# Kernel tuning notes

Hardware: AMD Instinct MI355X
Metric: run time of the kernel (lower is better)

## Reference

```python
import jax, jax.numpy as jnp
import numpy as np

DIM = 768
HEADS = 12
HEAD_DIM = DIM // HEADS
SCALE = HEAD_DIM ** (-0.5)


def setup_inputs() -> dict:
    key = jax.random.key(0)
    k1, k2, k3, k4 = jax.random.split(key, 4)
    B, N = 2, 48 * 48
    x = jax.random.normal(k1, (B, N, DIM), dtype=jnp.float32)
    qkv_w = jax.random.normal(k2, (3 * DIM, DIM), dtype=jnp.float32) * (DIM ** -0.5)
    proj_w = jax.random.normal(k3, (DIM, DIM), dtype=jnp.float32) * (DIM ** -0.5)
    proj_b = jax.random.normal(k4, (DIM,), dtype=jnp.float32) * 0.02
    return {"x": x, "H": 48, "W": 48, "qkv_w": qkv_w, "proj_w": proj_w, "proj_b": proj_b}


def reference(x, H, W, qkv_w, proj_w, proj_b):
    B, N, C = x.shape
    h, d = HEADS, HEAD_DIM
    # qkv linear (no bias): [B,N,3C], then split into per-head q,k,v [B,h,N,d]
    qkv = jnp.einsum('bnc,fc->bnf', x, qkv_w)
    qkv = qkv.reshape(B, N, 3, h, d).transpose(2, 0, 3, 1, 4)
    q, k, v = qkv[0], qkv[1], qkv[2]
    attn = jnp.einsum('bhnd,bhmd->bhnm', q, k) * SCALE  # [B,h,N,N]
    attn = jax.nn.softmax(attn, axis=-1)
    out = jnp.einsum('bhnm,bhmd->bhnd', attn, v)  # [B,h,N,d]
    out = out.transpose(0, 2, 1, 3).reshape(B, N, C)
    out = jnp.einsum('bnc,fc->bnf', out, proj_w) + proj_b
    return out
```

## Files before the change

### kernel.cpp

```cpp
#include <hip/hip_runtime.h>

#define B_    2
#define N_    2304
#define C_    768
#define HEADS 12
#define D_    64
#define F3    2304
#define M_    (B_*N_)
#define SPLITS 2
#define KSPAN (N_/SPLITS)
#define QSCALE 0.18033688011112042f

typedef __attribute__((ext_vector_type(8)))  short bfrag;
typedef __attribute__((ext_vector_type(4)))  float ffrag;
typedef __attribute__((ext_vector_type(16))) float ffrag16;
typedef __attribute__((ext_vector_type(4)))  unsigned ufrag;
typedef __attribute__((ext_vector_type(2)))  unsigned uint2v;

__device__ __forceinline__ short f2bf(float f) {
    unsigned u = __float_as_uint(f);
    u += 0x7fff + ((u >> 16) & 1);
    return (short)(u >> 16);
}

__device__ __forceinline__ void gl2lds16(const void* g, void* l) {
    __builtin_amdgcn_global_load_lds(
        (const __attribute__((address_space(1))) void*)g,
        (__attribute__((address_space(3))) void*)l, 16, 0, 0);
}

__device__ __forceinline__ void wait_vm4() { asm volatile("s_waitcnt vmcnt(4)" ::: "memory"); }
__device__ __forceinline__ void wait_vm0() { asm volatile("s_waitcnt vmcnt(0)" ::: "memory"); }

__device__ __forceinline__ unsigned pktrunc(float a, float b) {
    return __builtin_amdgcn_perm(__float_as_uint(a), __float_as_uint(b),
                                 0x03020706u);
}

__global__ __launch_bounds__(256) void cast_all(const float* __restrict__ x,
                                                const float* __restrict__ qw,
                                                const float* __restrict__ pw,
                                                short* __restrict__ dst) {
    const int nx4 = (M_*C_)/4, nq4 = (F3*C_)/4, np4 = (C_*C_)/4;
    int i = blockIdx.x * 256 + threadIdx.x;
    if (i >= nx4 + nq4 + np4) return;
    const float* src; int off;
    if (i < nx4)            { src = x;  off = i; }
    else if (i < nx4 + nq4) { src = qw; off = i - nx4; }
    else                    { src = pw; off = i - nx4 - nq4; }
    float4 v = ((const float4*)src)[off];
    short4 o;
    o.x = f2bf(v.x); o.y = f2bf(v.y); o.z = f2bf(v.z); o.w = f2bf(v.w);
    ((short4*)dst)[i] = o;
}

__global__ __launch_bounds__(256) void qkv_gemm(const short* __restrict__ xb,
                                                const short* __restrict__ wb,
                                                short* __restrict__ Qb,
                                                short* __restrict__ Kb,
                                                short* __restrict__ Vtb) {
    __shared__ short As[2][128*32];
    __shared__ short Bs[2][128*32];
    const int t = threadIdx.x;
    const int w = t >> 6, lane = t & 63;
    const int quad = lane >> 4, l15 = lane & 15;
    const int wr = w >> 1, wc = w & 1;

    const int nwg = gridDim.x * gridDim.y;
    const int bid = blockIdx.y * gridDim.x + blockIdx.x;
    const int swz = (bid & 7) * (nwg >> 3) + (bid >> 3);
    const int m0 = (swz / gridDim.x) * 128, f0 = (swz % gridDim.x) * 128;

    const int srow = lane >> 2;
    const int skk  = (lane & 3) * 8;

    ffrag acc[4][4] = {};

    #pragma unroll
    for (int r = 0; r < 2; ++r) {
        int seg = r*4 + w;
        int row = seg*16 + srow;
        gl2lds16(xb + (size_t)(m0+row)*C_ + skk, As[0] + seg*512);
        gl2lds16(wb + (size_t)(f0+row)*C_ + skk, Bs[0] + seg*512);
    }

    const int NKT = C_/32;
    for (int kt = 0; kt < NKT; ++kt) {
        const int cur = kt & 1;
        if (kt + 1 < NKT) {
            const int k0n = (kt+1)*32;
            #pragma unroll
            for (int r = 0; r < 2; ++r) {
                int seg = r*4 + w;
                int row = seg*16 + srow;
                gl2lds16(xb + (size_t)(m0+row)*C_ + k0n + skk, As[cur^1] + seg*512);
                gl2lds16(wb + (size_t)(f0+row)*C_ + k0n + skk, Bs[cur^1] + seg*512);
            }
            wait_vm4();
        } else {
            wait_vm0();
        }
        __builtin_amdgcn_s_barrier();

        bfrag af[4], bf[4];
        #pragma unroll
        for (int i = 0; i < 4; ++i)
            af[i] = *(const bfrag*)(As[cur] + (wr*64 + i*16 + l15)*32 + quad*8);
        #pragma unroll
        for (int j = 0; j < 4; ++j)
            bf[j] = *(const bfrag*)(Bs[cur] + (wc*64 + j*16 + l15)*32 + quad*8);
        #pragma unroll
        for (int i = 0; i < 4; ++i)
            #pragma unroll
            for (int j = 0; j < 4; ++j)
                acc[i][j] = __builtin_amdgcn_mfma_f32_16x16x32_bf16(af[i], bf[j], acc[i][j], 0, 0, 0);
        __builtin_amdgcn_s_barrier();
    }

    const int b   = m0 / N_;
    const int seg = f0 + wc*64;
    const int which = seg / C_;
    const int head  = (seg - which*C_) >> 6;
    const int bh    = b*HEADS + head;
    const int nbase = (m0 - b*N_) + wr*64 + quad*4;

    if (which == 0) {
        #pragma unroll
        for (int i = 0; i < 4; ++i) {
            int n0 = nbase + i*16;
            #pragma unroll
            for (int j = 0; j < 4; ++j) {
                int d = j*16 + l15;
                #pragma unroll
                for (int r = 0; r < 4; ++r)
                    Qb[((size_t)bh*N_ + n0 + r)*D_ + d] = f2bf(acc[i][j][r] * QSCALE);
            }
        }
    } else if (which == 1) {
        #pragma unroll
        for (int i = 0; i < 4; ++i) {
            int n0 = nbase + i*16;
            #pragma unroll
            for (int j = 0; j < 4; ++j) {
                int d = j*16 + l15;
                #pragma unroll
                for (int r = 0; r < 4; ++r)
                    Kb[((size_t)bh*N_ + n0 + r)*D_ + d] = f2bf(acc[i][j][r]);
            }
        }
    } else {
        #pragma unroll
        for (int i = 0; i < 4; ++i) {
            int n0 = nbase + i*16;
            #pragma unroll
            for (int j = 0; j < 4; ++j) {
                int d = j*16 + l15;
                short4 vv;
                vv.x = f2bf(acc[i][j][0]);
                vv.y = f2bf(acc[i][j][1]);
                vv.z = f2bf(acc[i][j][2]);
                vv.w = f2bf(acc[i][j][3]);
                *(short4*)(Vtb + ((size_t)bh*D_ + d)*N_ + n0) = vv;
            }
        }
    }
}

__global__ __launch_bounds__(256, 4) void attn_mfma(const short* __restrict__ Qb,
                                                    const short* __restrict__ Kb,
                                                    const short* __restrict__ Vtb,
                                                    float* __restrict__ Opart,
                                                    float* __restrict__ lpart) {
    __shared__ short lds[16384];
    const int t = threadIdx.x;
    const int w = t >> 6, lane = t & 63;
    const int l31 = lane & 31, hi = lane >> 5;

    const int nwg = gridDim.x * gridDim.y;
    const int fid = blockIdx.y * gridDim.x + blockIdx.x;
    const int swz = (fid & 7) * (nwg >> 3) + (fid >> 3);
    const int bh  = swz / gridDim.x;
    const int q0  = (swz - bh * gridDim.x) * 128;

    const int split = blockIdx.z;
    const int kbase = split * KSPAN;
    const size_t base = (size_t)bh * N_ * D_;
    const int lrow = lane >> 3;
    const int lc   = (lane & 7) ^ lrow;

    short* Qs = lds + 8192;

    #pragma unroll
    for (int r = 0; r < 4; ++r) {
        int s = r*4 + w;
        gl2lds16(Qb + base + (size_t)(q0 + s*8 + lrow)*D_ + lc*8, Qs + s*512);
    }
    #pragma unroll
    for (int r = 0; r < 2; ++r) {
        int s = r*4 + w;
        int row = s*8 + lrow;
        gl2lds16(Kb  + base + (size_t)(kbase+row)*D_ + lc*8,    lds + s*512);
        gl2lds16(Vtb + (size_t)(bh*D_ + row)*N_ + kbase + lc*8, lds + 4096 + s*512);
    }
    __syncthreads();

    bfrag qf[4];
    {
        int row = w*32 + l31, r7 = row & 7;
        #pragma unroll
        for (int kc = 0; kc < 4; ++kc)
            qf[kc] = *(const bfrag*)(Qs + row*64 + ((kc*2 + hi) ^ r7)*8);
    }
    __syncthreads();

    bfrag vones;
    #pragma unroll
    for (int j = 0; j < 8; ++j) vones[j] = (short)0x3f80;

    ffrag16 oacc[2], lfr;
    #pragma unroll
    for (int r = 0; r < 16; ++r) { oacc[0][r] = 0.f; oacc[1][r] = 0.f; lfr[r] = 0.f; }

    const int NT = KSPAN / 64;
    for (int ti = 0; ti < NT; ++ti) {
        const int cur = ti & 1;
        const short* Kc = lds + cur*8192;
        const short* Vc = Kc + 4096;

        if (ti + 1 < NT) {
            short* Kn = lds + (cur^1)*8192;
            const int k0n = kbase + (ti+1)*64;
            #pragma unroll
            for (int r = 0; r < 2; ++r) {
                int s = r*4 + w;
                int row = s*8 + lrow;
                gl2lds16(Kb  + base + (size_t)(k0n+row)*D_ + lc*8,    Kn + s*512);
                gl2lds16(Vtb + (size_t)(bh*D_ + row)*N_ + k0n + lc*8, Kn + 4096 + s*512);
            }
            wait_vm4();
        } else {
            wait_vm0();
        }
        __builtin_amdgcn_s_barrier();

        ufrag pfr[4];
        #pragma unroll
        for (int kt = 0; kt < 2; ++kt) {
            ffrag16 s;
            #pragma unroll
            for (int r = 0; r < 16; ++r) s[r] = 0.f;
            int row = kt*32 + l31, r7 = row & 7;
            __builtin_amdgcn_s_setprio(1);
            #pragma unroll
            for (int kc = 0; kc < 4; ++kc) {
                bfrag kf = *(const bfrag*)(Kc + row*64 + ((kc*2 + hi) ^ r7)*8);
                s = __builtin_amdgcn_mfma_f32_32x32x16_bf16(kf, qf[kc], s, 0, 0, 0);
            }
            __builtin_amdgcn_s_setprio(0);
            #pragma unroll
            for (int r = 0; r < 16; ++r)
                s[r] = __builtin_amdgcn_exp2f(s[r]);
            unsigned q01_0 = pktrunc(s[0],  s[1]),  q23_0 = pktrunc(s[2],  s[3]);
            unsigned q01_1 = pktrunc(s[4],  s[5]),  q23_1 = pktrunc(s[6],  s[7]);
            unsigned q01_2 = pktrunc(s[8],  s[9]),  q23_2 = pktrunc(s[10], s[11]);
            unsigned q01_3 = pktrunc(s[12], s[13]), q23_3 = pktrunc(s[14], s[15]);
            uint2v e0 = __builtin_amdgcn_permlane32_swap(q01_0, q01_1, false, false);
            uint2v e1 = __builtin_amdgcn_permlane32_swap(q23_0, q23_1, false, false);
            uint2v e2 = __builtin_amdgcn_permlane32_swap(q01_2, q01_3, false, false);
            uint2v e3 = __builtin_amdgcn_permlane32_swap(q23_2, q23_3, false, false);
            ufrag lo, hif;
            lo[0]  = e0[0]; lo[1]  = e1[0]; lo[2]  = e0[1]; lo[3]  = e1[1];
            hif[0] = e2[0]; hif[1] = e3[0]; hif[2] = e2[1]; hif[3] = e3[1];
            pfr[kt*2]     = lo;
            pfr[kt*2 + 1] = hif;
        }

        __builtin_amdgcn_s_setprio(1);
        #pragma unroll
        for (int kc = 0; kc < 4; ++kc) {
            bfrag pf = __builtin_bit_cast(bfrag, pfr[kc]);
            #pragma unroll
            for (int dt = 0; dt < 2; ++dt) {
                int row = dt*32 + l31, r7 = row & 7;
                bfrag vf = *(const bfrag*)(Vc + row*64 + ((kc*2 + hi) ^ r7)*8);
                oacc[dt] = __builtin_amdgcn_mfma_f32_32x32x16_bf16(pf, vf, oacc[dt], 0, 0, 0);
            }
            lfr = __builtin_amdgcn_mfma_f32_32x32x16_bf16(pf, vones, lfr, 0, 0, 0);
        }
        __builtin_amdgcn_s_setprio(0);
        __builtin_amdgcn_s_barrier();
    }

    const int b = bh / HEADS, head = bh - b*HEADS;
    float* Op = Opart + (size_t)split * M_ * C_;
    float* lp = lpart + (size_t)split * (B_*HEADS) * N_;

    if (l31 == 0) {
        #pragma unroll
        for (int r = 0; r < 16; ++r) {
            int n = q0 + w*32 + (r & 3) + 8*(r >> 2) + 4*hi;
            lp[bh*N_ + n] = lfr[r];
        }
    }

    #pragma unroll
    for (int dt = 0; dt < 2; ++dt)
        #pragma unroll
        for (int r = 0; r < 16; ++r) {
            int n = q0 + w*32 + (r & 3) + 8*(r >> 2) + 4*hi;
            int c = head*D_ + dt*32 + l31;
            Op[((size_t)b*N_ + n)*C_ + c] = oacc[dt][r];
        }
}

__global__ __launch_bounds__(256) void attn_merge(const float* __restrict__ Opart,
                                                  const float* __restrict__ lpart,
                                                  short* __restrict__ Ob) {
    int i = blockIdx.x * 256 + threadIdx.x;
    int m = i / (C_/4);
    int c = (i - m*(C_/4)) * 4;
    int b = m / N_, n = m - b*N_;
    int bh = b*HEADS + (c >> 6);
    float4 o0 = ((const float4*)Opart)[i];
    float4 o1 = ((const float4*)(Opart + (size_t)M_*C_))[i];
    float l = lpart[bh*N_ + n] + lpart[(B_*HEADS)*N_ + bh*N_ + n];
    float inv = 1.f / l;
    short4 o;
    o.x = f2bf((o0.x + o1.x) * inv);
    o.y = f2bf((o0.y + o1.y) * inv);
    o.z = f2bf((o0.z + o1.z) * inv);
    o.w = f2bf((o0.w + o1.w) * inv);
    ((short4*)Ob)[i] = o;
}

__global__ __launch_bounds__(256) void proj_gemm(const short* __restrict__ Ab,
                                                 const short* __restrict__ wb,
                                                 const float* __restrict__ bias,
                                                 float* __restrict__ out) {
    __shared__ short As[2][128*32];
    __shared__ short Bs[2][128*32];
    const int t = threadIdx.x;
    const int w = t >> 6, lane = t & 63;
    const int quad = lane >> 4, l15 = lane & 15;
    const int wr = w >> 1, wc = w & 1;

    const int nwg = gridDim.x * gridDim.y;
    const int bid = blockIdx.y * gridDim.x + blockIdx.x;
    const int swz = (bid & 7) * (nwg >> 3) + (bid >> 3);
    const int m0 = (swz / gridDim.x) * 128, f0 = (swz % gridDim.x) * 128;

    const int srow = lane >> 2;
    const int skk  = (lane & 3) * 8;

    ffrag acc[4][4] = {};

    #pragma unroll
    for (int r = 0; r < 2; ++r) {
        int seg = r*4 + w;
        int row = seg*16 + srow;
        gl2lds16(Ab + (size_t)(m0+row)*C_ + skk, As[0] + seg*512);
        gl2lds16(wb + (size_t)(f0+row)*C_ + skk, Bs[0] + seg*512);
    }

    const int NKT = C_/32;
    for (int kt = 0; kt < NKT; ++kt) {
        const int cur = kt & 1;
        if (kt + 1 < NKT) {
            const int k0n = (kt+1)*32;
            #pragma unroll
            for (int r = 0; r < 2; ++r) {
                int seg = r*4 + w;
                int row = seg*16 + srow;
                gl2lds16(Ab + (size_t)(m0+row)*C_ + k0n + skk, As[cur^1] + seg*512);
                gl2lds16(wb + (size_t)(f0+row)*C_ + k0n + skk, Bs[cur^1] + seg*512);
            }
            wait_vm4();
        } else {
            wait_vm0();
        }
        __builtin_amdgcn_s_barrier();

        bfrag af[4], bf[4];
        #pragma unroll
        for (int i = 0; i < 4; ++i)
            af[i] = *(const bfrag*)(As[cur] + (wr*64 + i*16 + l15)*32 + quad*8);
        #pragma unroll
        for (int j = 0; j < 4; ++j)
            bf[j] = *(const bfrag*)(Bs[cur] + (wc*64 + j*16 + l15)*32 + quad*8);
        #pragma unroll
        for (int i = 0; i < 4; ++i)
            #pragma unroll
            for (int j = 0; j < 4; ++j)
                acc[i][j] = __builtin_amdgcn_mfma_f32_16x16x32_bf16(af[i], bf[j], acc[i][j], 0, 0, 0);
        __builtin_amdgcn_s_barrier();
    }

    #pragma unroll
    for (int i = 0; i < 4; ++i) {
        int mbase = m0 + wr*64 + i*16 + quad*4;
        #pragma unroll
        for (int j = 0; j < 4; ++j) {
            int f = f0 + wc*64 + j*16 + l15;
            float bv = bias[f];
            #pragma unroll
            for (int r = 0; r < 4; ++r)
                out[(size_t)(mbase + r)*C_ + f] = acc[i][j][r] + bv;
        }
    }
}

extern "C" void kernel_launch(void* const* d_in, const int* in_sizes, int n_in,
                              void* d_out, int out_size, void* d_ws, size_t ws_size,
                              hipStream_t stream) {
    const float* x      = (const float*)d_in[0];
    const float* qkv_w  = (const float*)d_in[3];
    const float* proj_w = (const float*)d_in[4];
    const float* proj_b = (const float*)d_in[5];
    float* out = (float*)d_out;

    const size_t nx = (size_t)M_ * C_;
    const size_t nq = (size_t)F3 * C_;
    const size_t np = (size_t)C_ * C_;
    short* xb  = (short*)d_ws;
    short* qwb = xb  + nx;
    short* pwb = qwb + nq;
    short* Qb  = pwb + np;
    short* Kb  = Qb  + nx;
    short* Vtb = Kb  + nx;
    short* Ob  = Vtb + nx;
    float* Opart = (float*)(Ob + nx);
    float* lpart = Opart + (size_t)SPLITS * M_ * C_;

    const int ncast4 = (int)((nx + nq + np) / 4);
    cast_all<<<dim3((ncast4 + 255)/256), 256, 0, stream>>>(x, qkv_w, proj_w, xb);

    qkv_gemm<<<dim3(F3/128, M_/128), 256, 0, stream>>>(xb, qwb, Qb, Kb, Vtb);
    attn_mfma<<<dim3(N_/128, B_*HEADS, SPLITS), 256, 0, stream>>>(Qb, Kb, Vtb, Opart, lpart);
    attn_merge<<<dim3(((int)(nx/4) + 255)/256), 256, 0, stream>>>(Opart, lpart, Ob);
    proj_gemm<<<dim3(C_/128, M_/128), 256, 0, stream>>>(Ob, pwb, proj_b, out);
}
```

Baseline: 194.4 us.

## Software-pipeline attention loop to overlap QK/exp of next half with PV MFMAs

Restructures the attention inner loop so the second half-tile's QK^T, exp and packing, along with its V fragment loads into registers, are carried across the barrier and consumed in the next iteration. The PV MFMAs of the previous half then interleave with the current tile's QK and exp work. The first tile is peeled as a prologue and a final PV step is added as an epilogue. The goal is to hide exp/VALU latency behind matrix ops, at the cost of extra live registers (P and V fragments) under launch_bounds(256,4).

```diff
diff --git a/kernel.cpp b/kernel.cpp
--- a/kernel.cpp
+++ b/kernel.cpp
@@ -166,6 +166,83 @@
     }
 }
 
+
+__device__ __forceinline__ void qkpack(const short* Kc, const bfrag* qf,
+                                       int kt, int l31, int hi,
+                                       ufrag& u0, ufrag& u1) {
+    ffrag16 s;
+    #pragma unroll
+    for (int r = 0; r < 16; ++r) s[r] = 0.f;
+    int row = kt*32 + l31, r7 = row & 7;
+    __builtin_amdgcn_s_setprio(1);
+    #pragma unroll
+    for (int kc = 0; kc < 4; ++kc) {
+        bfrag kf = *(const bfrag*)(Kc + row*64 + ((kc*2 + hi) ^ r7)*8);
+        s = __builtin_amdgcn_mfma_f32_32x32x16_bf16(kf, qf[kc], s, 0, 0, 0);
+    }
+    __builtin_amdgcn_s_setprio(0);
+    #pragma unroll
+    for (int r = 0; r < 16; ++r)
+        s[r] = __builtin_amdgcn_exp2f(s[r]);
+    unsigned q01_0 = pktrunc(s[0],  s[1]),  q23_0 = pktrunc(s[2],  s[3]);
+    unsigned q01_1 = pktrunc(s[4],  s[5]),  q23_1 = pktrunc(s[6],  s[7]);
+    unsigned q01_2 = pktrunc(s[8],  s[9]),  q23_2 = pktrunc(s[10], s[11]);
+    unsigned q01_3 = pktrunc(s[12], s[13]), q23_3 = pktrunc(s[14], s[15]);
+    uint2v e0 = __builtin_amdgcn_permlane32_swap(q01_0, q01_1, false, false);
+    uint2v e1 = __builtin_amdgcn_permlane32_swap(q23_0, q23_1, false, false);
+    uint2v e2 = __builtin_amdgcn_permlane32_swap(q01_2, q01_3, false, false);
+    uint2v e3 = __builtin_amdgcn_permlane32_swap(q23_2, q23_3, false, false);
+    ufrag lo, hif;
+    lo[0]  = e0[0]; lo[1]  = e1[0]; lo[2]  = e0[1]; lo[3]  = e1[1];
+    hif[0] = e2[0]; hif[1] = e3[0]; hif[2] = e2[1]; hif[3] = e3[1];
+    u0 = lo; u1 = hif;
+}
+
+__device__ __forceinline__ void pv_lds(ufrag u0, ufrag u1, const short* Vc,
+                                       int kt, int l31, int hi, bfrag vones,
+                                       ffrag16& o0, ffrag16& o1, ffrag16& lf) {
+    int r0 = l31, r7a = r0 & 7;
+    int r1 = 32 + l31, r7b = r1 & 7;
+    bfrag p0 = __builtin_bit_cast(bfrag, u0);
+    bfrag p1 = __builtin_bit_cast(bfrag, u1);
+    int kcA = kt*2, kcB = kt*2 + 1;
+    bfrag vA0 = *(const bfrag*)(Vc + r0*64 + ((kcA*2 + hi) ^ r7a)*8);
+    bfrag vA1 = *(const bfrag*)(Vc + r1*64 + ((kcA*2 + hi) ^ r7b)*8);
+    bfrag vB0 = *(const bfrag*)(Vc + r0*64 + ((kcB*2 + hi) ^ r7a)*8);
+    bfrag vB1 = *(const bfrag*)(Vc + r1*64 + ((kcB*2 + hi) ^ r7b)*8);
+    o0 = __builtin_amdgcn_mfma_f32_32x32x16_bf16(p0, vA0, o0, 0, 0, 0);
+    o1 = __builtin_amdgcn_mfma_f32_32x32x16_bf16(p0, vA1, o1, 0, 0, 0);
+    lf = __builtin_amdgcn_mfma_f32_32x32x16_bf16(p0, vones, lf, 0, 0, 0);
+    o0 = __builtin_amdgcn_mfma_f32_32x32x16_bf16(p1, vB0, o0, 0, 0, 0);
+    o1 = __builtin_amdgcn_mfma_f32_32x32x16_bf16(p1, vB1, o1, 0, 0, 0);
+    lf = __builtin_amdgcn_mfma_f32_32x32x16_bf16(p1, vones, lf, 0, 0, 0);
+}
+
+__device__ __forceinline__ void pv_reg(ufrag u0, ufrag u1,
+                                       bfrag v0, bfrag v1, bfrag v2, bfrag v3,
+                                       bfrag vones,
+                                       ffrag16& o0, ffrag16& o1, ffrag16& lf) {
+    bfrag p0 = __builtin_bit_cast(bfrag, u0);
+    bfrag p1 = __builtin_bit_cast(bfrag, u1);
+    o0 = __builtin_amdgcn_mfma_f32_32x32x16_bf16(p0, v0, o0, 0, 0, 0);
+    o1 = __builtin_amdgcn_mfma_f32_32x32x16_bf16(p0, v1, o1, 0, 0, 0);
+    lf = __builtin_amdgcn_mfma_f32_32x32x16_bf16(p0, vones, lf, 0, 0, 0);
+    o0 = __builtin_amdgcn_mfma_f32_32x32x16_bf16(p1, v2, o0, 0, 0, 0);
+    o1 = __builtin_amdgcn_mfma_f32_32x32x16_bf16(p1, v3, o1, 0, 0, 0);
+    lf = __builtin_amdgcn_mfma_f32_32x32x16_bf16(p1, vones, lf, 0, 0, 0);
+}
+
+__device__ __forceinline__ void vload4(const short* Vc, int kt, int l31, int hi,
+                                       bfrag& v0, bfrag& v1, bfrag& v2, bfrag& v3) {
+    int r0 = l31, r7a = r0 & 7;
+    int r1 = 32 + l31, r7b = r1 & 7;
+    int kcA = kt*2, kcB = kt*2 + 1;
+    v0 = *(const bfrag*)(Vc + r0*64 + ((kcA*2 + hi) ^ r7a)*8);
+    v1 = *(const bfrag*)(Vc + r1*64 + ((kcA*2 + hi) ^ r7b)*8);
+    v2 = *(const bfrag*)(Vc + r0*64 + ((kcB*2 + hi) ^ r7a)*8);
+    v3 = *(const bfrag*)(Vc + r1*64 + ((kcB*2 + hi) ^ r7b)*8);
+}
+
 __global__ __launch_bounds__(256, 4) void attn_mfma(const short* __restrict__ Qb,
                                                     const short* __restrict__ Kb,
                                                     const short* __restrict__ Vtb,
@@ -217,12 +294,37 @@
     #pragma unroll
     for (int j = 0; j < 8; ++j) vones[j] = (short)0x3f80;
 
-    ffrag16 oacc[2], lfr;
-    #pragma unroll
-    for (int r = 0; r < 16; ++r) { oacc[0][r] = 0.f; oacc[1][r] = 0.f; lfr[r] = 0.f; }
+    ffrag16 oacc0, oacc1, lfr;
+    #pragma unroll
+    for (int r = 0; r < 16; ++r) { oacc0[r] = 0.f; oacc1[r] = 0.f; lfr[r] = 0.f; }
 
     const int NT = KSPAN / 64;
-    for (int ti = 0; ti < NT; ++ti) {
+
+    ufrag pP0, pP1;
+    bfrag vP0, vP1, vP2, vP3;
+
+    {
+        const int k0n = kbase + 64;
+        #pragma unroll
+        for (int r = 0; r < 2; ++r) {
+            int s = r*4 + w;
+            int row = s*8 + lrow;
+            gl2lds16(Kb  + base + (size_t)(k0n+row)*D_ + lc*8,    lds + 8192 + s*512);
+            gl2lds16(Vtb + (size_t)(bh*D_ + row)*N_ + k0n + lc*8, lds + 12288 + s*512);
+        }
+        const short* Kc = lds;
+        const short* Vc = lds + 4096;
+        ufrag a0, a1;
+        qkpack(Kc, qf, 0, l31, hi, a0, a1);
+        __builtin_amdgcn_s_setprio(1);
+        pv_lds(a0, a1, Vc, 0, l31, hi, vones, oacc0, oacc1, lfr);
+        __builtin_amdgcn_s_setprio(0);
+        qkpack(Kc, qf, 1, l31, hi, pP0, pP1);
+        vload4(Vc, 1, l31, hi, vP0, vP1, vP2, vP3);
+        __builtin_amdgcn_s_barrier();
+    }
+
+    for (int ti = 1; ti < NT; ++ti) {
         const int cur = ti & 1;
         const short* Kc = lds + cur*8192;
         const short* Vc = Kc + 4096;
@@ -243,53 +345,18 @@
         }
         __builtin_amdgcn_s_barrier();
 
-        ufrag pfr[4];
-        #pragma unroll
-        for (int kt = 0; kt < 2; ++kt) {
-            ffrag16 s;
-            #pragma unroll
-            for (int r = 0; r < 16; ++r) s[r] = 0.f;
-            int row = kt*32 + l31, r7 = row & 7;
-            __builtin_amdgcn_s_setprio(1);
-            #pragma unroll
-            for (int kc = 0; kc < 4; ++kc) {
-                bfrag kf = *(const bfrag*)(Kc + row*64 + ((kc*2 + hi) ^ r7)*8);
-                s = __builtin_amdgcn_mfma_f32_32x32x16_bf16(kf, qf[kc], s, 0, 0, 0);
-            }
-            __builtin_amdgcn_s_setprio(0);
-            #pragma unroll
-            for (int r = 0; r < 16; ++r)
-                s[r] = __builtin_amdgcn_exp2f(s[r]);
-            unsigned q01_0 = pktrunc(s[0],  s[1]),  q23_0 = pktrunc(s[2],  s[3]);
-            unsigned q01_1 = pktrunc(s[4],  s[5]),  q23_1 = pktrunc(s[6],  s[7]);
-            unsigned q01_2 = pktrunc(s[8],  s[9]),  q23_2 = pktrunc(s[10], s[11]);
-            unsigned q01_3 = pktrunc(s[12], s[13]), q23_3 = pktrunc(s[14], s[15]);
-            uint2v e0 = __builtin_amdgcn_permlane32_swap(q01_0, q01_1, false, false);
-            uint2v e1 = __builtin_amdgcn_permlane32_swap(q23_0, q23_1, false, false);
-            uint2v e2 = __builtin_amdgcn_permlane32_swap(q01_2, q01_3, false, false);
-            uint2v e3 = __builtin_amdgcn_permlane32_swap(q23_2, q23_3, false, false);
-            ufrag lo, hif;
-            lo[0]  = e0[0]; lo[1]  = e1[0]; lo[2]  = e0[1]; lo[3]  = e1[1];
-            hif[0] = e2[0]; hif[1] = e3[0]; hif[2] = e2[1]; hif[3] = e3[1];
-            pfr[kt*2]     = lo;
-            pfr[kt*2 + 1] = hif;
-        }
-
+        ufrag a0, a1;
+        qkpack(Kc, qf, 0, l31, hi, a0, a1);
         __builtin_amdgcn_s_setprio(1);
-        #pragma unroll
-        for (int kc = 0; kc < 4; ++kc) {
-            bfrag pf = __builtin_bit_cast(bfrag, pfr[kc]);
-            #pragma unroll
-            for (int dt = 0; dt < 2; ++dt) {
-                int row = dt*32 + l31, r7 = row & 7;
-                bfrag vf = *(const bfrag*)(Vc + row*64 + ((kc*2 + hi) ^ r7)*8);
-                oacc[dt] = __builtin_amdgcn_mfma_f32_32x32x16_bf16(pf, vf, oacc[dt], 0, 0, 0);
-            }
-            lfr = __builtin_amdgcn_mfma_f32_32x32x16_bf16(pf, vones, lfr, 0, 0, 0);
-        }
+        pv_reg(pP0, pP1, vP0, vP1, vP2, vP3, vones, oacc0, oacc1, lfr);
+        pv_lds(a0, a1, Vc, 0, l31, hi, vones, oacc0, oacc1, lfr);
         __builtin_amdgcn_s_setprio(0);
-        __builtin_amdgcn_s_barrier();
-    }
+        qkpack(Kc, qf, 1, l31, hi, pP0, pP1);
+        vload4(Vc, 1, l31, hi, vP0, vP1, vP2, vP3);
+        __builtin_amdgcn_s_barrier();
+    }
+
+    pv_reg(pP0, pP1, vP0, vP1, vP2, vP3, vones, oacc0, oacc1, lfr);
 
     const int b = bh / HEADS, head = bh - b*HEADS;
     float* Op = Opart + (size_t)split * M_ * C_;
@@ -304,13 +371,12 @@
     }
 
     #pragma unroll
-    for (int dt = 0; dt < 2; ++dt)
-        #pragma unroll
-        for (int r = 0; r < 16; ++r) {
-            int n = q0 + w*32 + (r & 3) + 8*(r >> 2) + 4*hi;
-            int c = head*D_ + dt*32 + l31;
-            Op[((size_t)b*N_ + n)*C_ + c] = oacc[dt][r];
-        }
+    for (int r = 0; r < 16; ++r) {
+        int n = q0 + w*32 + (r & 3) + 8*(r >> 2) + 4*hi;
+        int c = head*D_ + l31;
+        Op[((size_t)b*N_ + n)*C_ + c] = oacc0[r];
+        Op[((size_t)b*N_ + n)*C_ + c + 32] = oacc1[r];
+    }
 }
 
 __global__ __launch_bounds__(256) void attn_merge(const float* __restrict__ Opart,
```

Measured after the change: 193.3 us. Within noise of the previous version (-0.6%).
